# Performance work log

Hardware: AMD Instinct MI355X
Metric: run time of the kernel (lower is better)

## Reference

```python
import jax, jax.numpy as jnp
import numpy as np

B, U, V = 4, 64, 256
IN_DIM, STATE_DIM, CODE_DIM = 768, 768, 384
NUM_HEADS, HEAD_DIM = 8, 64
INNER = NUM_HEADS * HEAD_DIM  # 512
SCALE = HEAD_DIM ** 0.5


def _ln(x, g, b, eps=1e-5):
    mu = jnp.mean(x, axis=-1, keepdims=True)
    var = jnp.var(x, axis=-1, keepdims=True)
    return (x - mu) * jax.lax.rsqrt(var + eps) * g + b


def setup_inputs() -> dict:
    key = jax.random.key(0)
    ks = jax.random.split(key, 12)
    def w(k, shape, s=0.02):
        return jax.random.normal(k, shape, jnp.float32) * s
    return {
        "receiver_states": jax.random.normal(ks[0], (B, U, STATE_DIM), jnp.float32),
        "receiver_codes": jax.random.normal(ks[1], (B, U, CODE_DIM), jnp.float32),
        "sender_states": jax.random.normal(ks[2], (B, V, IN_DIM), jnp.float32),
        "ln_r_g": jnp.ones((STATE_DIM,), jnp.float32),
        "ln_r_b": jnp.zeros((STATE_DIM,), jnp.float32),
        "ln_s_g": jnp.ones((IN_DIM,), jnp.float32),
        "ln_s_b": jnp.zeros((IN_DIM,), jnp.float32),
        "Wq": w(ks[3], (STATE_DIM, INNER)), "bq": jnp.zeros((INNER,), jnp.float32), "Wmq": w(ks[4], (CODE_DIM, STATE_DIM)),
        "Wk": w(ks[5], (IN_DIM, INNER)),   "bk": jnp.zeros((INNER,), jnp.float32), "Wmk": w(ks[6], (CODE_DIM, IN_DIM)),
        "Wv": w(ks[7], (IN_DIM, INNER)),   "bv": jnp.zeros((INNER,), jnp.float32), "Wmv": w(ks[8], (CODE_DIM, IN_DIM)),
        "We": w(ks[9], (INNER, STATE_DIM)), "be": jnp.zeros((STATE_DIM,), jnp.float32), "Wme": w(ks[10], (CODE_DIM, INNER)),
        "gamma": jnp.ones((STATE_DIM,), jnp.float32),  # LayerScale, init 1.0
    }


def reference(receiver_states, receiver_codes, sender_states,
              ln_r_g, ln_r_b, ln_s_g, ln_s_b,
              Wq, bq, Wmq, Wk, bk, Wmk, Wv, bv, Wmv, We, be, Wme, gamma):
    r = _ln(receiver_states, ln_r_g, ln_r_b)   # (b,u,ds)
    s = _ln(sender_states, ln_s_g, ln_s_b)     # (b,v,di)
    # ModFC: y = (x * (1 + ctx @ Wm)) @ W + b  (code-conditioned input modulation)
    q = (r * (1.0 + receiver_codes @ Wmq)) @ Wq + bq          # (b,u,inner)
    mk = 1.0 + receiver_codes @ Wmk                           # (b,u,di)
    mv = 1.0 + receiver_codes @ Wmv                           # (b,u,di)
    xs = s[:, :, None, :]                                     # (b,v,1,di)
    k = (xs * mk[:, None, :, :]) @ Wk + bk                    # (b,v,u,inner)
    v = (xs * mv[:, None, :, :]) @ Wv + bv                    # (b,v,u,inner)
    qh = q.reshape(B, U, NUM_HEADS, HEAD_DIM)
    kh = k.reshape(B, V, U, NUM_HEADS, HEAD_DIM)
    vh = v.reshape(B, V, U, NUM_HEADS, HEAD_DIM)
    scores = jnp.einsum('buhc,bvuhc->bhuv', qh, kh) / SCALE   # (b,h,u,v)
    weights = jax.nn.softmax(scores, axis=-1)
    msg = jnp.einsum('bhuv,bvuhc->buhc', weights, vh).reshape(B, U, INNER)
    out = (msg * (1.0 + receiver_codes @ Wme)) @ We + be      # exit ModFC -> (b,u,ds)
    out = out * gamma                                         # LayerScale
    return receiver_states + out                              # residual
```

## Files before the change

kernel.cpp:

```cpp
#include <hip/hip_runtime.h>


#define DD 768
#define CDIM 384
#define NH 8
#define HD 64
#define INNER 512
#define VV 256

typedef unsigned short u16;

__device__ __forceinline__ void fma4(float4& a, float s, const float4& b) {
  a.x += s * b.x; a.y += s * b.y; a.z += s * b.z; a.w += s * b.w;
}

__device__ __forceinline__ float4 bexp(uint2 u) {
  float4 r;
  r.x = __uint_as_float(u.x << 16);
  r.y = __uint_as_float(u.x & 0xffff0000u);
  r.z = __uint_as_float(u.y << 16);
  r.w = __uint_as_float(u.y & 0xffff0000u);
  return r;
}

__device__ __forceinline__ u16 f2b(float v) {
  return (u16)((__float_as_uint(v) + 0x8000u) >> 16);
}

template <int K, int NS>
__device__ __forceinline__ void gcore(const float* __restrict__ A0, int lda,
                                      const float* __restrict__ Bp,
                                      float4& a0, float4& a1, float4& a2,
                                      float4& a3) {
  float4 b0[8], b1[8];
#pragma unroll
  for (int i = 0; i < 8; i++) b0[i] = *(const float4*)(Bp + (size_t)i * NS);
  const float* Bq = Bp + (size_t)8 * NS;
#pragma unroll 1
  for (int kk = 0; kk < K; kk += 16) {
#pragma unroll
    for (int i = 0; i < 8; i++) b1[i] = *(const float4*)(Bq + (size_t)i * NS);
    Bq += (size_t)8 * NS;
#pragma unroll
    for (int c = 0; c < 2; c++) {
      int kb = kk + c * 4;
      float4 f0 = *(const float4*)(A0 + kb);
      float4 f1 = *(const float4*)(A0 + lda + kb);
      float4 f2 = *(const float4*)(A0 + 2 * lda + kb);
      float4 f3 = *(const float4*)(A0 + 3 * lda + kb);
      float4 bv;
      bv = b0[c*4+0]; fma4(a0,f0.x,bv); fma4(a1,f1.x,bv); fma4(a2,f2.x,bv); fma4(a3,f3.x,bv);
      bv = b0[c*4+1]; fma4(a0,f0.y,bv); fma4(a1,f1.y,bv); fma4(a2,f2.y,bv); fma4(a3,f3.y,bv);
      bv = b0[c*4+2]; fma4(a0,f0.z,bv); fma4(a1,f1.z,bv); fma4(a2,f2.z,bv); fma4(a3,f3.z,bv);
      bv = b0[c*4+3]; fma4(a0,f0.w,bv); fma4(a1,f1.w,bv); fma4(a2,f2.w,bv); fma4(a3,f3.w,bv);
    }
    if (kk + 16 < K) {
#pragma unroll
      for (int i = 0; i < 8; i++) b0[i] = *(const float4*)(Bq + (size_t)i * NS);
      Bq += (size_t)8 * NS;
    }
#pragma unroll
    for (int c = 0; c < 2; c++) {
      int kb = kk + 8 + c * 4;
      float4 f0 = *(const float4*)(A0 + kb);
      float4 f1 = *(const float4*)(A0 + lda + kb);
      float4 f2 = *(const float4*)(A0 + 2 * lda + kb);
      float4 f3 = *(const float4*)(A0 + 3 * lda + kb);
      float4 bv;
      bv = b1[c*4+0]; fma4(a0,f0.x,bv); fma4(a1,f1.x,bv); fma4(a2,f2.x,bv); fma4(a3,f3.x,bv);
      bv = b1[c*4+1]; fma4(a0,f0.y,bv); fma4(a1,f1.y,bv); fma4(a2,f2.y,bv); fma4(a3,f3.y,bv);
      bv = b1[c*4+2]; fma4(a0,f0.z,bv); fma4(a1,f1.z,bv); fma4(a2,f2.z,bv); fma4(a3,f3.z,bv);
      bv = b1[c*4+3]; fma4(a0,f0.w,bv); fma4(a1,f1.w,bv); fma4(a2,f2.w,bv); fma4(a3,f3.w,bv);
    }
  }
}

template <int K, int NS>
__device__ __forceinline__ void gcoreb(const float* __restrict__ A0, int lda,
                                       const u16* __restrict__ Bp,
                                       float4& a0, float4& a1, float4& a2,
                                       float4& a3) {
  uint2 b0[8], b1[8];
#pragma unroll
  for (int i = 0; i < 8; i++) b0[i] = *(const uint2*)(Bp + (size_t)i * NS);
  const u16* Bq = Bp + (size_t)8 * NS;
#pragma unroll 1
  for (int kk = 0; kk < K; kk += 16) {
#pragma unroll
    for (int i = 0; i < 8; i++) b1[i] = *(const uint2*)(Bq + (size_t)i * NS);
    Bq += (size_t)8 * NS;
#pragma unroll
    for (int c = 0; c < 2; c++) {
      int kb = kk + c * 4;
      float4 f0 = *(const float4*)(A0 + kb);
      float4 f1 = *(const float4*)(A0 + lda + kb);
      float4 f2 = *(const float4*)(A0 + 2 * lda + kb);
      float4 f3 = *(const float4*)(A0 + 3 * lda + kb);
      float4 bv;
      bv = bexp(b0[c*4+0]); fma4(a0,f0.x,bv); fma4(a1,f1.x,bv); fma4(a2,f2.x,bv); fma4(a3,f3.x,bv);
      bv = bexp(b0[c*4+1]); fma4(a0,f0.y,bv); fma4(a1,f1.y,bv); fma4(a2,f2.y,bv); fma4(a3,f3.y,bv);
      bv = bexp(b0[c*4+2]); fma4(a0,f0.z,bv); fma4(a1,f1.z,bv); fma4(a2,f2.z,bv); fma4(a3,f3.z,bv);
      bv = bexp(b0[c*4+3]); fma4(a0,f0.w,bv); fma4(a1,f1.w,bv); fma4(a2,f2.w,bv); fma4(a3,f3.w,bv);
    }
    if (kk + 16 < K) {
#pragma unroll
      for (int i = 0; i < 8; i++) b0[i] = *(const uint2*)(Bq + (size_t)i * NS);
      Bq += (size_t)8 * NS;
    }
#pragma unroll
    for (int c = 0; c < 2; c++) {
      int kb = kk + 8 + c * 4;
      float4 f0 = *(const float4*)(A0 + kb);
      float4 f1 = *(const float4*)(A0 + lda + kb);
      float4 f2 = *(const float4*)(A0 + 2 * lda + kb);
      float4 f3 = *(const float4*)(A0 + 3 * lda + kb);
      float4 bv;
      bv = bexp(b1[c*4+0]); fma4(a0,f0.x,bv); fma4(a1,f1.x,bv); fma4(a2,f2.x,bv); fma4(a3,f3.x,bv);
      bv = bexp(b1[c*4+1]); fma4(a0,f0.y,bv); fma4(a1,f1.y,bv); fma4(a2,f2.y,bv); fma4(a3,f3.y,bv);
      bv = bexp(b1[c*4+2]); fma4(a0,f0.z,bv); fma4(a1,f1.z,bv); fma4(a2,f2.z,bv); fma4(a3,f3.z,bv);
      bv = bexp(b1[c*4+3]); fma4(a0,f0.w,bv); fma4(a1,f1.w,bv); fma4(a2,f2.w,bv); fma4(a3,f3.w,bv);
    }
  }
}


__global__ __launch_bounds__(256) void k_s0(
    const float* __restrict__ Wmq, const float* __restrict__ Wmk,
    const float* __restrict__ Wmv, const float* __restrict__ Wme,
    const float* __restrict__ Wq, const float* __restrict__ Wk,
    const float* __restrict__ Wv, const float* __restrict__ We,
    u16* __restrict__ bw) {
  __shared__ float TL[64 * 65];
  int bid = blockIdx.x, t = threadIdx.x;
  if (bid < 96) {
    int d0 = (bid >> 3) * 64, c0 = (bid & 7) * 64;
    int j = t & 63, i0 = t >> 6;
#pragma unroll
    for (int p = 0; p < 16; p++) {
      int i = p * 4 + i0;
      TL[i * 65 + j] = Wk[(size_t)(d0 + i) * INNER + c0 + j];
    }
    __syncthreads();
    u16* dst = bw + 2260992;
#pragma unroll
    for (int p = 0; p < 16; p++) {
      int i = p * 4 + i0;
      dst[(size_t)(c0 + i) * DD + d0 + j] = f2b(TL[j * 65 + i]);
    }
  } else {
    for (int idx = (bid - 96) * 256 + t; idx < 565248; idx += 1184 * 256) {
      const float* src; u16* dst; int off;
      if (idx < 73728)       { src = Wmq; dst = bw;           off = idx; }
      else if (idx < 147456) { src = Wmk; dst = bw + 294912;  off = idx - 73728; }
      else if (idx < 221184) { src = Wmv; dst = bw + 589824;  off = idx - 147456; }
      else if (idx < 270336) { src = Wme; dst = bw + 884736;  off = idx - 221184; }
      else if (idx < 368640) { src = Wq;  dst = bw + 1081344; off = idx - 270336; }
      else if (idx < 466944) { src = Wv;  dst = bw + 1474560; off = idx - 368640; }
      else                   { src = We;  dst = bw + 1867776; off = idx - 466944; }
      float4 v = *(const float4*)(src + (size_t)off * 4);
      ushort4 o;
      o.x = f2b(v.x); o.y = f2b(v.y); o.z = f2b(v.z); o.w = f2b(v.w);
      *(ushort4*)(dst + (size_t)off * 4) = o;
    }
  }
}

__global__ __launch_bounds__(256, 2) void k_s1(
    const float* __restrict__ ss, const float* __restrict__ rs,
    const float* __restrict__ g_s, const float* __restrict__ b_s,
    const float* __restrict__ g_r, const float* __restrict__ b_r,
    const float* __restrict__ codes, const u16* __restrict__ bw,
    float* __restrict__ s_ln, float* __restrict__ r_ln,
    float* __restrict__ cp) {
  __shared__ __align__(16) float SB[6400];
  int bid = blockIdx.x, t = threadIdx.x;
  if (bid < 176) {
    int nc = bid % 11, mb = bid / 11;
    int base = nc * 256;
    const u16* W; int N, colW;
    if (base < 768)       { W = bw;          N = DD;    colW = base; }
    else if (base < 1536) { W = bw + 294912; N = DD;    colW = base - 768; }
    else if (base < 2304) { W = bw + 589824; N = DD;    colW = base - 1536; }
    else                  { W = bw + 884736; N = INNER; colW = base - 2304; }
    int m0 = mb * 16;
#pragma unroll
    for (int p = 0; p < 24; p++) {
      int idx = p * 256 + t, r = idx / 384, k = idx % 384;
      SB[idx] = codes[(size_t)(m0 + r) * CDIM + k];
    }
    __syncthreads();
    int kl = t & 63, wid = t >> 6;
    const float* A0 = SB + (wid * 4) * 384;
    float4 a0 = {0,0,0,0}, a1 = {0,0,0,0}, a2 = {0,0,0,0}, a3 = {0,0,0,0};
    if (N == DD)
      gcoreb<384, DD>(A0, 384, W + colW + 4 * kl, a0, a1, a2, a3);
    else
      gcoreb<384, INNER>(A0, 384, W + colW + 4 * kl, a0, a1, a2, a3);
    int m = m0 + wid * 4, gcol = base + 4 * kl;
    *(float4*)(cp + (size_t)m * 2816 + gcol) = a0;
    *(float4*)(cp + (size_t)(m + 1) * 2816 + gcol) = a1;
    *(float4*)(cp + (size_t)(m + 2) * 2816 + gcol) = a2;
    *(float4*)(cp + (size_t)(m + 3) * 2816 + gcol) = a3;
  } else {
    int rr = bid - 176;
    const float *x, *g, *bb; float* y; int r;
    if (rr < 1024) { x = ss; g = g_s; bb = b_s; y = s_ln; r = rr; }
    else           { x = rs; g = g_r; bb = b_r; y = r_ln; r = rr - 1024; }
    const float* xr = x + (size_t)r * DD;
    float v0 = xr[t], v1 = xr[t + 256], v2 = xr[t + 512];
    float s = v0 + v1 + v2, sq = v0 * v0 + v1 * v1 + v2 * v2;
    for (int o = 32; o > 0; o >>= 1) {
      s += __shfl_down(s, o, 64); sq += __shfl_down(sq, o, 64);
    }
    int wid = t >> 6, lane = t & 63;
    if (lane == 0) { SB[wid] = s; SB[wid + 4] = sq; }
    __syncthreads();
    float sum = SB[0] + SB[1] + SB[2] + SB[3];
    float ssq = SB[4] + SB[5] + SB[6] + SB[7];
    float mu = sum * (1.0f / 768.0f);
    float var = ssq * (1.0f / 768.0f) - mu * mu;
    float rstd = rsqrtf(var + 1e-5f);
    float* yr = y + (size_t)r * DD;
    yr[t]       = (v0 - mu) * rstd * g[t]       + bb[t];
    yr[t + 256] = (v1 - mu) * rstd * g[t + 256] + bb[t + 256];
    yr[t + 512] = (v2 - mu) * rstd * g[t + 512] + bb[t + 512];
  }
}

__global__ __launch_bounds__(256, 2) void k_s2(
    const float* __restrict__ s_ln, const float* __restrict__ r_ln,
    const float* __restrict__ cp, const u16* __restrict__ bw,
    float* __restrict__ sT, float* __restrict__ qp) {
  __shared__ __align__(16) float SB[4160];
  int bid = blockIdx.x, t = threadIdx.x;
  if (bid < 128) {
    int ks = bid & 3, t2 = bid >> 2, nc = t2 & 1, mb = t2 >> 1;
    int m0 = mb * 16, col0 = nc * 256, k0 = ks * 192;
#pragma unroll
    for (int p = 0; p < 12; p++) {
      int idx = p * 256 + t, r = idx / 192, k = idx % 192;
      int d = k0 + k;
      float mqv = cp[(size_t)(m0 + r) * 2816 + d] + 1.0f;
      SB[idx] = r_ln[(size_t)(m0 + r) * DD + d] * mqv;
    }
    __syncthreads();
    int kl = t & 63, wid = t >> 6;
    int col = col0 + 4 * kl;
    const float* A0 = SB + (wid * 4) * 192;
    float4 a0 = {0,0,0,0}, a1 = {0,0,0,0}, a2 = {0,0,0,0}, a3 = {0,0,0,0};
    gcoreb<192, INNER>(A0, 192, bw + 1081344 + (size_t)k0 * INNER + col,
                       a0, a1, a2, a3);
    int m = m0 + wid * 4;
    float* dst = qp + (size_t)ks * (256 * INNER);
    *(float4*)(dst + (size_t)m * INNER + col) = a0;
    *(float4*)(dst + (size_t)(m + 1) * INNER + col) = a1;
    *(float4*)(dst + (size_t)(m + 2) * INNER + col) = a2;
    *(float4*)(dst + (size_t)(m + 3) * INNER + col) = a3;
  } else {
    int tid = bid - 128;
    int vt = tid & 3, dt = (tid >> 2) % 12, b = tid / 48;
    int v0 = vt * 64, d0 = dt * 64;
    int j = t & 63, i0 = t >> 6;
#pragma unroll
    for (int p = 0; p < 16; p++) {
      int i = p * 4 + i0;
      SB[i * 65 + j] = s_ln[(size_t)(b * VV + v0 + i) * DD + d0 + j];
    }
    __syncthreads();
#pragma unroll
    for (int p = 0; p < 16; p++) {
      int i = p * 4 + i0;
      sT[((size_t)b * DD + d0 + i) * VV + v0 + j] = SB[j * 65 + i];
    }
  }
}

__global__ __launch_bounds__(256, 2) void k_s3(
    const float* __restrict__ qp, const float* __restrict__ bq,
    const u16* __restrict__ bw, const float* __restrict__ cp,
    const float* __restrict__ bk, float* __restrict__ qm,
    float* __restrict__ qbk) {
  __shared__ __align__(16) float SB[1024];
  int bid = blockIdx.x, t = threadIdx.x;
  if (bid < 384) {
    int h = bid & 7, dc = (bid >> 3) % 3, mb = bid / 24;
    int m0 = mb * 16;
#pragma unroll
    for (int p = 0; p < 4; p++) {
      int idx = p * 256 + t, r = idx >> 6, c = idx & 63;
      int i = h * HD + c;
      size_t off = (size_t)(m0 + r) * INNER + i;
      SB[idx] = qp[off] + qp[131072 + off] + qp[262144 + off] +
                qp[393216 + off] + bq[i];
    }
    __syncthreads();
    int kl = t & 63, wid = t >> 6;
    int col = dc * 256 + 4 * kl;
    const float* A0 = SB + (wid * 4) * HD;
    float4 a0 = {0,0,0,0}, a1 = {0,0,0,0}, a2 = {0,0,0,0}, a3 = {0,0,0,0};
    gcoreb<64, DD>(A0, HD, bw + 2260992 + (size_t)(h * HD) * DD + col,
                   a0, a1, a2, a3);
#pragma unroll
    for (int j = 0; j < 4; j++) {
      float4 a = (j == 0) ? a0 : (j == 1) ? a1 : (j == 2) ? a2 : a3;
      int m = m0 + wid * 4 + j;
      const float* mkp = cp + (size_t)m * 2816 + 768 + col;
      float4 o = {a.x * (mkp[0] + 1.0f), a.y * (mkp[1] + 1.0f),
                  a.z * (mkp[2] + 1.0f), a.w * (mkp[3] + 1.0f)};
      *(float4*)(qm + ((size_t)m * NH + h) * DD + col) = o;
    }
  } else {
    int m = bid - 384;
    size_t off = (size_t)m * INNER;
    SB[t] = (qp[off + t] + qp[131072 + off + t] + qp[262144 + off + t] +
             qp[393216 + off + t] + bq[t]) * bk[t];
    int t2 = t + 256;
    SB[t2] = (qp[off + t2] + qp[131072 + off + t2] + qp[262144 + off + t2] +
              qp[393216 + off + t2] + bq[t2]) * bk[t2];
    __syncthreads();
    if (t < 8) {
      float a = 0.f;
      for (int c = 0; c < HD; c++) a += SB[t * HD + c];
      qbk[m * NH + t] = a;
    }
  }
}

__global__ __launch_bounds__(256, 2) void k_s4(
    const float* __restrict__ qm, const float* __restrict__ sT,
    float* __restrict__ scp) {
  __shared__ __align__(16) float SB[3072];
  int bid = blockIdx.x, t = threadIdx.x;
  int ks = bid & 3, b = (bid >> 2) & 3, mb = bid >> 4;
  int gi0 = b * 512 + mb * 16, k0 = ks * 192;
#pragma unroll
  for (int p = 0; p < 12; p++) {
    int idx = p * 256 + t, r = idx / 192, k = idx % 192;
    SB[idx] = qm[(size_t)(gi0 + r) * DD + k0 + k];
  }
  __syncthreads();
  int kl = t & 63, wid = t >> 6;
  int col = 4 * kl;
  const float* A0 = SB + (wid * 4) * 192;
  float4 a0 = {0,0,0,0}, a1 = {0,0,0,0}, a2 = {0,0,0,0}, a3 = {0,0,0,0};
  gcore<192, VV>(A0, 192, sT + ((size_t)b * DD + k0) * VV + col, a0, a1, a2, a3);
  int gi = gi0 + wid * 4;
  float* dst = scp + (size_t)ks * (2048 * VV);
  *(float4*)(dst + (size_t)gi * VV + col) = a0;
  *(float4*)(dst + (size_t)(gi + 1) * VV + col) = a1;
  *(float4*)(dst + (size_t)(gi + 2) * VV + col) = a2;
  *(float4*)(dst + (size_t)(gi + 3) * VV + col) = a3;
}

__global__ __launch_bounds__(256, 2) void k_s5(
    const float* __restrict__ scp, const float* __restrict__ qbk,
    const float* __restrict__ s_ln, const float* __restrict__ cp,
    float* __restrict__ wsm) {
  __shared__ __align__(16) float SB[4096];
  int bid = blockIdx.x, t = threadIdx.x;
  int dc = bid % 3, up = (bid / 3) % 32, b = bid / 96;
  int gi0 = b * 512 + up * 16;
#pragma unroll
  for (int p = 0; p < 16; p++) {
    int idx = p * 256 + t, r = idx >> 8, c = idx & 255;
    size_t o = (size_t)(gi0 + r) * VV + c;
    float v = scp[o] + scp[524288 + o] + scp[1048576 + o] + scp[1572864 + o];
    int m = b * 64 + up * 2 + (r >> 3), h = r & 7;
    SB[idx] = (v + qbk[m * NH + h]) * 0.125f;
  }
  __syncthreads();
  int wid = t >> 6, lane = t & 63;
#pragma unroll
  for (int j = 0; j < 4; j++) {
    int r = wid * 4 + j;
    float x0 = SB[r * 256 + lane],       x1 = SB[r * 256 + lane + 64];
    float x2 = SB[r * 256 + lane + 128], x3 = SB[r * 256 + lane + 192];
    float mx = fmaxf(fmaxf(x0, x1), fmaxf(x2, x3));
    for (int o = 1; o < 64; o <<= 1) mx = fmaxf(mx, __shfl_xor(mx, o, 64));
    float e0 = __expf(x0 - mx), e1 = __expf(x1 - mx);
    float e2 = __expf(x2 - mx), e3 = __expf(x3 - mx);
    float sm = e0 + e1 + e2 + e3;
    for (int o = 1; o < 64; o <<= 1) sm += __shfl_xor(sm, o, 64);
    float rinv = 1.0f / sm;
    SB[r * 256 + lane] = e0 * rinv;       SB[r * 256 + lane + 64] = e1 * rinv;
    SB[r * 256 + lane + 128] = e2 * rinv; SB[r * 256 + lane + 192] = e3 * rinv;
  }
  __syncthreads();
  int kl = t & 63;
  int col = dc * 256 + 4 * kl;
  const float* A0 = SB + (wid * 4) * 256;
  float4 a0 = {0,0,0,0}, a1 = {0,0,0,0}, a2 = {0,0,0,0}, a3 = {0,0,0,0};
  gcore<VV, DD>(A0, 256, s_ln + (size_t)(b * VV) * DD + col, a0, a1, a2, a3);
#pragma unroll
  for (int j = 0; j < 4; j++) {
    float4 a = (j == 0) ? a0 : (j == 1) ? a1 : (j == 2) ? a2 : a3;
    int r = wid * 4 + j;
    int ul = r >> 3, h = r & 7, m = b * 64 + up * 2 + ul;
    const float* mvp = cp + (size_t)m * 2816 + 1536 + col;
    float4 o = {a.x * (mvp[0] + 1.0f), a.y * (mvp[1] + 1.0f),
                a.z * (mvp[2] + 1.0f), a.w * (mvp[3] + 1.0f)};
    *(float4*)(wsm + ((size_t)h * 256 + m) * DD + col) = o;
  }
}

__global__ __launch_bounds__(256, 2) void k_s6(
    const float* __restrict__ wsm, const u16* __restrict__ bw,
    float* __restrict__ mmp) {
  __shared__ __align__(16) float SB[6400];
  int bid = blockIdx.x, t = threadIdx.x;
  int hp = bid & 1, ks = (bid >> 1) & 7, mb = bid >> 4;
  int h0 = hp * 4, m0 = mb * 16, k0 = ks * 96;
#pragma unroll
  for (int p = 0; p < 24; p++) {
    int idx = p * 256 + t;
    int e = idx / 1536, rem = idx % 1536, r = rem / 96, k = rem % 96;
    SB[e * 1540 + r * 96 + k] =
        wsm[((size_t)(h0 + e) * 256 + m0 + r) * DD + k0 + k];
  }
  __syncthreads();
  int kl = t & 63, wid = t >> 6;
  int hs = kl >> 4, c4 = 4 * (kl & 15);
  int colg = h0 * HD + hs * HD + c4;
  const float* A0 = SB + hs * 1540 + (wid * 4) * 96;
  float4 a0 = {0,0,0,0}, a1 = {0,0,0,0}, a2 = {0,0,0,0}, a3 = {0,0,0,0};
  gcoreb<96, INNER>(A0, 96, bw + 1474560 + (size_t)k0 * INNER + colg,
                    a0, a1, a2, a3);
  float* dst = mmp + (size_t)ks * (256 * INNER);
  int m = m0 + wid * 4;
  *(float4*)(dst + (size_t)m * INNER + colg) = a0;
  *(float4*)(dst + (size_t)(m + 1) * INNER + colg) = a1;
  *(float4*)(dst + (size_t)(m + 2) * INNER + colg) = a2;
  *(float4*)(dst + (size_t)(m + 3) * INNER + colg) = a3;
}

__global__ __launch_bounds__(256, 2) void k_s7(
    const float* __restrict__ mmp, const float* __restrict__ bvv,
    const float* __restrict__ cp, const u16* __restrict__ bw,
    float* __restrict__ op) {
  __shared__ __align__(16) float SB[1024];
  int bid = blockIdx.x, t = threadIdx.x;
  int ks = bid & 7, dc = (bid >> 3) % 3, mb = bid / 24;
  int m0 = mb * 16, k0 = ks * 64;
#pragma unroll
  for (int p = 0; p < 4; p++) {
    int idx = p * 256 + t, r = idx >> 6, k = idx & 63;
    int i = k0 + k;
    size_t off = (size_t)(m0 + r) * INNER + i;
    float v = mmp[off] + mmp[131072 + off] + mmp[262144 + off] +
              mmp[393216 + off] + mmp[524288 + off] + mmp[655360 + off] +
              mmp[786432 + off] + mmp[917504 + off];
    float mev = cp[(size_t)(m0 + r) * 2816 + 2304 + i] + 1.0f;
    SB[idx] = (v + bvv[i]) * mev;
  }
  __syncthreads();
  int kl = t & 63, wid = t >> 6;
  int col = dc * 256 + 4 * kl;
  const float* A0 = SB + (wid * 4) * 64;
  float4 a0 = {0,0,0,0}, a1 = {0,0,0,0}, a2 = {0,0,0,0}, a3 = {0,0,0,0};
  gcoreb<64, DD>(A0, 64, bw + 1867776 + (size_t)k0 * DD + col, a0, a1, a2, a3);
  float* dst = op + (size_t)ks * (256 * DD);
  int m = m0 + wid * 4;
  *(float4*)(dst + (size_t)m * DD + col) = a0;
  *(float4*)(dst + (size_t)(m + 1) * DD + col) = a1;
  *(float4*)(dst + (size_t)(m + 2) * DD + col) = a2;
  *(float4*)(dst + (size_t)(m + 3) * DD + col) = a3;
}

__global__ __launch_bounds__(256) void k_s8(
    const float* __restrict__ op, const float* __restrict__ be,
    const float* __restrict__ gamma, const float* __restrict__ rs,
    float* __restrict__ outp) {
  int m = blockIdx.x, t = threadIdx.x;
#pragma unroll
  for (int j = 0; j < 3; j++) {
    int d = t + j * 256;
    size_t off = (size_t)m * DD + d;
    float v = op[off] + op[196608 + off] + op[393216 + off] +
              op[589824 + off] + op[786432 + off] + op[983040 + off] +
              op[1179648 + off] + op[1376256 + off];
    outp[off] = rs[off] + (v + be[d]) * gamma[d];
  }
}

extern "C" void kernel_launch(void* const* d_in, const int* in_sizes, int n_in,
                              void* d_out, int out_size, void* d_ws, size_t ws_size,
                              hipStream_t stream) {
  const float* rs     = (const float*)d_in[0];
  const float* codes  = (const float*)d_in[1];
  const float* ss     = (const float*)d_in[2];
  const float* ln_r_g = (const float*)d_in[3];
  const float* ln_r_b = (const float*)d_in[4];
  const float* ln_s_g = (const float*)d_in[5];
  const float* ln_s_b = (const float*)d_in[6];
  const float* Wq  = (const float*)d_in[7];
  const float* bq  = (const float*)d_in[8];
  const float* Wmq = (const float*)d_in[9];
  const float* Wk  = (const float*)d_in[10];
  const float* bk  = (const float*)d_in[11];
  const float* Wmk = (const float*)d_in[12];
  const float* Wv  = (const float*)d_in[13];
  const float* bv  = (const float*)d_in[14];
  const float* Wmv = (const float*)d_in[15];
  const float* We  = (const float*)d_in[16];
  const float* be  = (const float*)d_in[17];
  const float* Wme = (const float*)d_in[18];
  const float* gamma = (const float*)d_in[19];

  float* w = (float*)d_ws;
  float* s_ln = w;
  float* r_ln = w + 786432;
  float* qp   = w + 1376256;
  float* sT   = w + 1900544;
  float* cp   = w + 2686976;
  float* qbk  = w + 3407872;
  float* qm   = w + 3409920;
  float* scp  = w + 4982784;
  float* wsm  = qm;
  float* mmp  = r_ln;
  float* op   = scp;
  u16*   bw   = (u16*)(w + 7079936);

  k_s0<<<dim3(1280), 256, 0, stream>>>(Wmq, Wmk, Wmv, Wme, Wq, Wk, Wv, We, bw);
  k_s1<<<dim3(1456), 256, 0, stream>>>(ss, rs, ln_s_g, ln_s_b, ln_r_g, ln_r_b,
                                       codes, bw, s_ln, r_ln, cp);
  k_s2<<<dim3(320), 256, 0, stream>>>(s_ln, r_ln, cp, bw, sT, qp);
  k_s3<<<dim3(640), 256, 0, stream>>>(qp, bq, bw, cp, bk, qm, qbk);
  k_s4<<<dim3(512), 256, 0, stream>>>(qm, sT, scp);
  k_s5<<<dim3(384), 256, 0, stream>>>(scp, qbk, s_ln, cp, wsm);
  k_s6<<<dim3(256), 256, 0, stream>>>(wsm, bw, mmp);
  k_s7<<<dim3(384), 256, 0, stream>>>(mmp, bv, cp, bw, op);
  k_s8<<<dim3(256), 256, 0, stream>>>(op, be, gamma, rs, (float*)d_out);
}
```

Measured before the change: 204.7 us.

## Halve per-block row tiles and fold weight conversion into first kernel

Each GEMM-style kernel now computes 2 rows per wave instead of 4, doubling the grid sizes of the stages to put more blocks on the many CUs. The separate weight-to-bf16 conversion kernel is merged into k_s1, and the code-modulation GEMM now reads fp32 weights directly and stores 1+x, so later stages drop their +1.0. This removes a launch and a dependency, but each block gets less register reuse of the loaded B vectors and more redundant B traffic.

```diff
diff --git a/kernel.cpp b/kernel.cpp
--- a/kernel.cpp
+++ b/kernel.cpp
@@ -28,10 +28,9 @@
 }
 
 template <int K, int NS>
-__device__ __forceinline__ void gcore(const float* __restrict__ A0, int lda,
-                                      const float* __restrict__ Bp,
-                                      float4& a0, float4& a1, float4& a2,
-                                      float4& a3) {
+__device__ __forceinline__ void gcore2(const float* __restrict__ A0, int lda,
+                                       const float* __restrict__ Bp,
+                                       float4& a0, float4& a1) {
   float4 b0[8], b1[8];
 #pragma unroll
   for (int i = 0; i < 8; i++) b0[i] = *(const float4*)(Bp + (size_t)i * NS);
@@ -46,13 +45,11 @@
       int kb = kk + c * 4;
       float4 f0 = *(const float4*)(A0 + kb);
       float4 f1 = *(const float4*)(A0 + lda + kb);
-      float4 f2 = *(const float4*)(A0 + 2 * lda + kb);
-      float4 f3 = *(const float4*)(A0 + 3 * lda + kb);
       float4 bv;
-      bv = b0[c*4+0]; fma4(a0,f0.x,bv); fma4(a1,f1.x,bv); fma4(a2,f2.x,bv); fma4(a3,f3.x,bv);
-      bv = b0[c*4+1]; fma4(a0,f0.y,bv); fma4(a1,f1.y,bv); fma4(a2,f2.y,bv); fma4(a3,f3.y,bv);
-      bv = b0[c*4+2]; fma4(a0,f0.z,bv); fma4(a1,f1.z,bv); fma4(a2,f2.z,bv); fma4(a3,f3.z,bv);
-      bv = b0[c*4+3]; fma4(a0,f0.w,bv); fma4(a1,f1.w,bv); fma4(a2,f2.w,bv); fma4(a3,f3.w,bv);
+      bv = b0[c*4+0]; fma4(a0, f0.x, bv); fma4(a1, f1.x, bv);
+      bv = b0[c*4+1]; fma4(a0, f0.y, bv); fma4(a1, f1.y, bv);
+      bv = b0[c*4+2]; fma4(a0, f0.z, bv); fma4(a1, f1.z, bv);
+      bv = b0[c*4+3]; fma4(a0, f0.w, bv); fma4(a1, f1.w, bv);
     }
     if (kk + 16 < K) {
 #pragma unroll
@@ -64,22 +61,19 @@
       int kb = kk + 8 + c * 4;
       float4 f0 = *(const float4*)(A0 + kb);
       float4 f1 = *(const float4*)(A0 + lda + kb);
-      float4 f2 = *(const float4*)(A0 + 2 * lda + kb);
-      float4 f3 = *(const float4*)(A0 + 3 * lda + kb);
       float4 bv;
-      bv = b1[c*4+0]; fma4(a0,f0.x,bv); fma4(a1,f1.x,bv); fma4(a2,f2.x,bv); fma4(a3,f3.x,bv);
-      bv = b1[c*4+1]; fma4(a0,f0.y,bv); fma4(a1,f1.y,bv); fma4(a2,f2.y,bv); fma4(a3,f3.y,bv);
-      bv = b1[c*4+2]; fma4(a0,f0.z,bv); fma4(a1,f1.z,bv); fma4(a2,f2.z,bv); fma4(a3,f3.z,bv);
-      bv = b1[c*4+3]; fma4(a0,f0.w,bv); fma4(a1,f1.w,bv); fma4(a2,f2.w,bv); fma4(a3,f3.w,bv);
+      bv = b1[c*4+0]; fma4(a0, f0.x, bv); fma4(a1, f1.x, bv);
+      bv = b1[c*4+1]; fma4(a0, f0.y, bv); fma4(a1, f1.y, bv);
+      bv = b1[c*4+2]; fma4(a0, f0.z, bv); fma4(a1, f1.z, bv);
+      bv = b1[c*4+3]; fma4(a0, f0.w, bv); fma4(a1, f1.w, bv);
     }
   }
 }
 
 template <int K, int NS>
-__device__ __forceinline__ void gcoreb(const float* __restrict__ A0, int lda,
-                                       const u16* __restrict__ Bp,
-                                       float4& a0, float4& a1, float4& a2,
-                                       float4& a3) {
+__device__ __forceinline__ void gcore2b(const float* __restrict__ A0, int lda,
+                                        const u16* __restrict__ Bp,
+                                        float4& a0, float4& a1) {
   uint2 b0[8], b1[8];
 #pragma unroll
   for (int i = 0; i < 8; i++) b0[i] = *(const uint2*)(Bp + (size_t)i * NS);
@@ -94,13 +88,11 @@
       int kb = kk + c * 4;
       float4 f0 = *(const float4*)(A0 + kb);
       float4 f1 = *(const float4*)(A0 + lda + kb);
-      float4 f2 = *(const float4*)(A0 + 2 * lda + kb);
-      float4 f3 = *(const float4*)(A0 + 3 * lda + kb);
       float4 bv;
-      bv = bexp(b0[c*4+0]); fma4(a0,f0.x,bv); fma4(a1,f1.x,bv); fma4(a2,f2.x,bv); fma4(a3,f3.x,bv);
-      bv = bexp(b0[c*4+1]); fma4(a0,f0.y,bv); fma4(a1,f1.y,bv); fma4(a2,f2.y,bv); fma4(a3,f3.y,bv);
-      bv = bexp(b0[c*4+2]); fma4(a0,f0.z,bv); fma4(a1,f1.z,bv); fma4(a2,f2.z,bv); fma4(a3,f3.z,bv);
-      bv = bexp(b0[c*4+3]); fma4(a0,f0.w,bv); fma4(a1,f1.w,bv); fma4(a2,f2.w,bv); fma4(a3,f3.w,bv);
+      bv = bexp(b0[c*4+0]); fma4(a0, f0.x, bv); fma4(a1, f1.x, bv);
+      bv = bexp(b0[c*4+1]); fma4(a0, f0.y, bv); fma4(a1, f1.y, bv);
+      bv = bexp(b0[c*4+2]); fma4(a0, f0.z, bv); fma4(a1, f1.z, bv);
+      bv = bexp(b0[c*4+3]); fma4(a0, f0.w, bv); fma4(a1, f1.w, bv);
     }
     if (kk + 16 < K) {
 #pragma unroll
@@ -112,97 +104,85 @@
       int kb = kk + 8 + c * 4;
       float4 f0 = *(const float4*)(A0 + kb);
       float4 f1 = *(const float4*)(A0 + lda + kb);
-      float4 f2 = *(const float4*)(A0 + 2 * lda + kb);
-      float4 f3 = *(const float4*)(A0 + 3 * lda + kb);
       float4 bv;
-      bv = bexp(b1[c*4+0]); fma4(a0,f0.x,bv); fma4(a1,f1.x,bv); fma4(a2,f2.x,bv); fma4(a3,f3.x,bv);
-      bv = bexp(b1[c*4+1]); fma4(a0,f0.y,bv); fma4(a1,f1.y,bv); fma4(a2,f2.y,bv); fma4(a3,f3.y,bv);
-      bv = bexp(b1[c*4+2]); fma4(a0,f0.z,bv); fma4(a1,f1.z,bv); fma4(a2,f2.z,bv); fma4(a3,f3.z,bv);
-      bv = bexp(b1[c*4+3]); fma4(a0,f0.w,bv); fma4(a1,f1.w,bv); fma4(a2,f2.w,bv); fma4(a3,f3.w,bv);
-    }
-  }
-}
-
-
-__global__ __launch_bounds__(256) void k_s0(
-    const float* __restrict__ Wmq, const float* __restrict__ Wmk,
-    const float* __restrict__ Wmv, const float* __restrict__ Wme,
-    const float* __restrict__ Wq, const float* __restrict__ Wk,
-    const float* __restrict__ Wv, const float* __restrict__ We,
-    u16* __restrict__ bw) {
-  __shared__ float TL[64 * 65];
-  int bid = blockIdx.x, t = threadIdx.x;
-  if (bid < 96) {
-    int d0 = (bid >> 3) * 64, c0 = (bid & 7) * 64;
+      bv = bexp(b1[c*4+0]); fma4(a0, f0.x, bv); fma4(a1, f1.x, bv);
+      bv = bexp(b1[c*4+1]); fma4(a0, f0.y, bv); fma4(a1, f1.y, bv);
+      bv = bexp(b1[c*4+2]); fma4(a0, f0.z, bv); fma4(a1, f1.z, bv);
+      bv = bexp(b1[c*4+3]); fma4(a0, f0.w, bv); fma4(a1, f1.w, bv);
+    }
+  }
+}
+
+
+__global__ __launch_bounds__(256, 2) void k_s1(
+    const float* __restrict__ ss, const float* __restrict__ rs,
+    const float* __restrict__ g_s, const float* __restrict__ b_s,
+    const float* __restrict__ g_r, const float* __restrict__ b_r,
+    const float* __restrict__ codes, const float* __restrict__ Wmq,
+    const float* __restrict__ Wmk, const float* __restrict__ Wmv,
+    const float* __restrict__ Wme, const float* __restrict__ Wk,
+    const float* __restrict__ Wq, const float* __restrict__ Wv,
+    const float* __restrict__ We,
+    float* __restrict__ s_ln, float* __restrict__ r_ln,
+    float* __restrict__ cp, u16* __restrict__ bw) {
+  __shared__ __align__(16) float SB[4160];
+  int bid = blockIdx.x, t = threadIdx.x;
+  if (bid < 352) {
+    int nc = bid % 11, mb = bid / 11;
+    int base = nc * 256;
+    const float* W; int N, colW;
+    if (base < 768)       { W = Wmq; N = DD;    colW = base; }
+    else if (base < 1536) { W = Wmk; N = DD;    colW = base - 768; }
+    else if (base < 2304) { W = Wmv; N = DD;    colW = base - 1536; }
+    else                  { W = Wme; N = INNER; colW = base - 2304; }
+    int m0 = mb * 8;
+#pragma unroll
+    for (int p = 0; p < 12; p++) {
+      int idx = p * 256 + t, r = idx / 384, k = idx % 384;
+      SB[idx] = codes[(size_t)(m0 + r) * CDIM + k];
+    }
+    __syncthreads();
+    int kl = t & 63, wid = t >> 6;
+    const float* A0 = SB + (wid * 2) * 384;
+    float4 a0 = {0,0,0,0}, a1 = {0,0,0,0};
+    if (N == DD)
+      gcore2<384, DD>(A0, 384, W + colW + 4 * kl, a0, a1);
+    else
+      gcore2<384, INNER>(A0, 384, W + colW + 4 * kl, a0, a1);
+    int m = m0 + wid * 2, gcol = base + 4 * kl;
+    float4 o0 = {1.f + a0.x, 1.f + a0.y, 1.f + a0.z, 1.f + a0.w};
+    float4 o1 = {1.f + a1.x, 1.f + a1.y, 1.f + a1.z, 1.f + a1.w};
+    *(float4*)(cp + (size_t)m * 2816 + gcol) = o0;
+    *(float4*)(cp + (size_t)(m + 1) * 2816 + gcol) = o1;
+  } else if (bid < 448) {
+    int tid = bid - 352;
+    int d0 = (tid >> 3) * 64, c0 = (tid & 7) * 64;
     int j = t & 63, i0 = t >> 6;
 #pragma unroll
     for (int p = 0; p < 16; p++) {
       int i = p * 4 + i0;
-      TL[i * 65 + j] = Wk[(size_t)(d0 + i) * INNER + c0 + j];
-    }
-    __syncthreads();
-    u16* dst = bw + 2260992;
+      SB[i * 65 + j] = Wk[(size_t)(d0 + i) * INNER + c0 + j];
+    }
+    __syncthreads();
+    u16* dst = bw + 1179648;
 #pragma unroll
     for (int p = 0; p < 16; p++) {
       int i = p * 4 + i0;
-      dst[(size_t)(c0 + i) * DD + d0 + j] = f2b(TL[j * 65 + i]);
-    }
-  } else {
-    for (int idx = (bid - 96) * 256 + t; idx < 565248; idx += 1184 * 256) {
+      dst[(size_t)(c0 + i) * DD + d0 + j] = f2b(SB[j * 65 + i]);
+    }
+  } else if (bid < 896) {
+    for (int idx = (bid - 448) * 256 + t; idx < 294912; idx += 448 * 256) {
       const float* src; u16* dst; int off;
-      if (idx < 73728)       { src = Wmq; dst = bw;           off = idx; }
-      else if (idx < 147456) { src = Wmk; dst = bw + 294912;  off = idx - 73728; }
-      else if (idx < 221184) { src = Wmv; dst = bw + 589824;  off = idx - 147456; }
-      else if (idx < 270336) { src = Wme; dst = bw + 884736;  off = idx - 221184; }
-      else if (idx < 368640) { src = Wq;  dst = bw + 1081344; off = idx - 270336; }
-      else if (idx < 466944) { src = Wv;  dst = bw + 1474560; off = idx - 368640; }
-      else                   { src = We;  dst = bw + 1867776; off = idx - 466944; }
+      if (idx < 98304)       { src = Wq; dst = bw;          off = idx; }
+      else if (idx < 196608) { src = Wv; dst = bw + 393216; off = idx - 98304; }
+      else                   { src = We; dst = bw + 786432; off = idx - 196608; }
       float4 v = *(const float4*)(src + (size_t)off * 4);
       ushort4 o;
       o.x = f2b(v.x); o.y = f2b(v.y); o.z = f2b(v.z); o.w = f2b(v.w);
       *(ushort4*)(dst + (size_t)off * 4) = o;
     }
-  }
-}
-
-__global__ __launch_bounds__(256, 2) void k_s1(
-    const float* __restrict__ ss, const float* __restrict__ rs,
-    const float* __restrict__ g_s, const float* __restrict__ b_s,
-    const float* __restrict__ g_r, const float* __restrict__ b_r,
-    const float* __restrict__ codes, const u16* __restrict__ bw,
-    float* __restrict__ s_ln, float* __restrict__ r_ln,
-    float* __restrict__ cp) {
-  __shared__ __align__(16) float SB[6400];
-  int bid = blockIdx.x, t = threadIdx.x;
-  if (bid < 176) {
-    int nc = bid % 11, mb = bid / 11;
-    int base = nc * 256;
-    const u16* W; int N, colW;
-    if (base < 768)       { W = bw;          N = DD;    colW = base; }
-    else if (base < 1536) { W = bw + 294912; N = DD;    colW = base - 768; }
-    else if (base < 2304) { W = bw + 589824; N = DD;    colW = base - 1536; }
-    else                  { W = bw + 884736; N = INNER; colW = base - 2304; }
-    int m0 = mb * 16;
-#pragma unroll
-    for (int p = 0; p < 24; p++) {
-      int idx = p * 256 + t, r = idx / 384, k = idx % 384;
-      SB[idx] = codes[(size_t)(m0 + r) * CDIM + k];
-    }
-    __syncthreads();
-    int kl = t & 63, wid = t >> 6;
-    const float* A0 = SB + (wid * 4) * 384;
-    float4 a0 = {0,0,0,0}, a1 = {0,0,0,0}, a2 = {0,0,0,0}, a3 = {0,0,0,0};
-    if (N == DD)
-      gcoreb<384, DD>(A0, 384, W + colW + 4 * kl, a0, a1, a2, a3);
-    else
-      gcoreb<384, INNER>(A0, 384, W + colW + 4 * kl, a0, a1, a2, a3);
-    int m = m0 + wid * 4, gcol = base + 4 * kl;
-    *(float4*)(cp + (size_t)m * 2816 + gcol) = a0;
-    *(float4*)(cp + (size_t)(m + 1) * 2816 + gcol) = a1;
-    *(float4*)(cp + (size_t)(m + 2) * 2816 + gcol) = a2;
-    *(float4*)(cp + (size_t)(m + 3) * 2816 + gcol) = a3;
   } else {
-    int rr = bid - 176;
+    int rr = bid - 896;
     const float *x, *g, *bb; float* y; int r;
     if (rr < 1024) { x = ss; g = g_s; bb = b_s; y = s_ln; r = rr; }
     else           { x = rs; g = g_r; bb = b_r; y = r_ln; r = rr - 1024; }
@@ -233,31 +213,27 @@
     float* __restrict__ sT, float* __restrict__ qp) {
   __shared__ __align__(16) float SB[4160];
   int bid = blockIdx.x, t = threadIdx.x;
-  if (bid < 128) {
+  if (bid < 256) {
     int ks = bid & 3, t2 = bid >> 2, nc = t2 & 1, mb = t2 >> 1;
-    int m0 = mb * 16, col0 = nc * 256, k0 = ks * 192;
-#pragma unroll
-    for (int p = 0; p < 12; p++) {
+    int m0 = mb * 8, col0 = nc * 256, k0 = ks * 192;
+#pragma unroll
+    for (int p = 0; p < 6; p++) {
       int idx = p * 256 + t, r = idx / 192, k = idx % 192;
       int d = k0 + k;
-      float mqv = cp[(size_t)(m0 + r) * 2816 + d] + 1.0f;
-      SB[idx] = r_ln[(size_t)(m0 + r) * DD + d] * mqv;
+      SB[idx] = r_ln[(size_t)(m0 + r) * DD + d] * cp[(size_t)(m0 + r) * 2816 + d];
     }
     __syncthreads();
     int kl = t & 63, wid = t >> 6;
     int col = col0 + 4 * kl;
-    const float* A0 = SB + (wid * 4) * 192;
-    float4 a0 = {0,0,0,0}, a1 = {0,0,0,0}, a2 = {0,0,0,0}, a3 = {0,0,0,0};
-    gcoreb<192, INNER>(A0, 192, bw + 1081344 + (size_t)k0 * INNER + col,
-                       a0, a1, a2, a3);
-    int m = m0 + wid * 4;
+    const float* A0 = SB + (wid * 2) * 192;
+    float4 a0 = {0,0,0,0}, a1 = {0,0,0,0};
+    gcore2b<192, INNER>(A0, 192, bw + (size_t)k0 * INNER + col, a0, a1);
+    int m = m0 + wid * 2;
     float* dst = qp + (size_t)ks * (256 * INNER);
     *(float4*)(dst + (size_t)m * INNER + col) = a0;
     *(float4*)(dst + (size_t)(m + 1) * INNER + col) = a1;
-    *(float4*)(dst + (size_t)(m + 2) * INNER + col) = a2;
-    *(float4*)(dst + (size_t)(m + 3) * INNER + col) = a3;
   } else {
-    int tid = bid - 128;
+    int tid = bid - 256;
     int vt = tid & 3, dt = (tid >> 2) % 12, b = tid / 48;
     int v0 = vt * 64, d0 = dt * 64;
     int j = t & 63, i0 = t >> 6;
@@ -280,13 +256,13 @@
     const u16* __restrict__ bw, const float* __restrict__ cp,
     const float* __restrict__ bk, float* __restrict__ qm,
     float* __restrict__ qbk) {
-  __shared__ __align__(16) float SB[1024];
-  int bid = blockIdx.x, t = threadIdx.x;
-  if (bid < 384) {
+  __shared__ __align__(16) float SB[512];
+  int bid = blockIdx.x, t = threadIdx.x;
+  if (bid < 768) {
     int h = bid & 7, dc = (bid >> 3) % 3, mb = bid / 24;
-    int m0 = mb * 16;
-#pragma unroll
-    for (int p = 0; p < 4; p++) {
+    int m0 = mb * 8;
+#pragma unroll
+    for (int p = 0; p < 2; p++) {
       int idx = p * 256 + t, r = idx >> 6, c = idx & 63;
       int i = h * HD + c;
       size_t off = (size_t)(m0 + r) * INNER + i;
@@ -296,31 +272,32 @@
     __syncthreads();
     int kl = t & 63, wid = t >> 6;
     int col = dc * 256 + 4 * kl;
-    const float* A0 = SB + (wid * 4) * HD;
-    float4 a0 = {0,0,0,0}, a1 = {0,0,0,0}, a2 = {0,0,0,0}, a3 = {0,0,0,0};
-    gcoreb<64, DD>(A0, HD, bw + 2260992 + (size_t)(h * HD) * DD + col,
-                   a0, a1, a2, a3);
-#pragma unroll
-    for (int j = 0; j < 4; j++) {
-      float4 a = (j == 0) ? a0 : (j == 1) ? a1 : (j == 2) ? a2 : a3;
-      int m = m0 + wid * 4 + j;
+    const float* A0 = SB + (wid * 2) * HD;
+    float4 a0 = {0,0,0,0}, a1 = {0,0,0,0};
+    gcore2b<64, DD>(A0, HD, bw + 1179648 + (size_t)(h * HD) * DD + col, a0, a1);
+#pragma unroll
+    for (int j = 0; j < 2; j++) {
+      float4 a = (j == 0) ? a0 : a1;
+      int m = m0 + wid * 2 + j;
       const float* mkp = cp + (size_t)m * 2816 + 768 + col;
-      float4 o = {a.x * (mkp[0] + 1.0f), a.y * (mkp[1] + 1.0f),
-                  a.z * (mkp[2] + 1.0f), a.w * (mkp[3] + 1.0f)};
+      float4 o = {a.x * mkp[0], a.y * mkp[1], a.z * mkp[2], a.w * mkp[3]};
       *(float4*)(qm + ((size_t)m * NH + h) * DD + col) = o;
     }
   } else {
-    int m = bid - 384;
+    int m = bid - 768;
     size_t off = (size_t)m * INNER;
-    SB[t] = (qp[off + t] + qp[131072 + off + t] + qp[262144 + off + t] +
-             qp[393216 + off + t] + bq[t]) * bk[t];
+    SB[t & 255] = 0.f;
+    float va = (qp[off + t] + qp[131072 + off + t] + qp[262144 + off + t] +
+                qp[393216 + off + t] + bq[t]) * bk[t];
     int t2 = t + 256;
-    SB[t2] = (qp[off + t2] + qp[131072 + off + t2] + qp[262144 + off + t2] +
-              qp[393216 + off + t2] + bq[t2]) * bk[t2];
+    float vb = (qp[off + t2] + qp[131072 + off + t2] + qp[262144 + off + t2] +
+                qp[393216 + off + t2] + bq[t2]) * bk[t2];
+    __shared__ float RED[512];
+    RED[t] = va; RED[t2] = vb;
     __syncthreads();
     if (t < 8) {
       float a = 0.f;
-      for (int c = 0; c < HD; c++) a += SB[t * HD + c];
+      for (int c = 0; c < HD; c++) a += RED[t * HD + c];
       qbk[m * NH + t] = a;
     }
   }
@@ -329,52 +306,49 @@
 __global__ __launch_bounds__(256, 2) void k_s4(
     const float* __restrict__ qm, const float* __restrict__ sT,
     float* __restrict__ scp) {
-  __shared__ __align__(16) float SB[3072];
+  __shared__ __align__(16) float SB[1536];
   int bid = blockIdx.x, t = threadIdx.x;
   int ks = bid & 3, b = (bid >> 2) & 3, mb = bid >> 4;
-  int gi0 = b * 512 + mb * 16, k0 = ks * 192;
-#pragma unroll
-  for (int p = 0; p < 12; p++) {
+  int gi0 = b * 512 + mb * 8, k0 = ks * 192;
+#pragma unroll
+  for (int p = 0; p < 6; p++) {
     int idx = p * 256 + t, r = idx / 192, k = idx % 192;
     SB[idx] = qm[(size_t)(gi0 + r) * DD + k0 + k];
   }
   __syncthreads();
   int kl = t & 63, wid = t >> 6;
   int col = 4 * kl;
-  const float* A0 = SB + (wid * 4) * 192;
-  float4 a0 = {0,0,0,0}, a1 = {0,0,0,0}, a2 = {0,0,0,0}, a3 = {0,0,0,0};
-  gcore<192, VV>(A0, 192, sT + ((size_t)b * DD + k0) * VV + col, a0, a1, a2, a3);
-  int gi = gi0 + wid * 4;
+  const float* A0 = SB + (wid * 2) * 192;
+  float4 a0 = {0,0,0,0}, a1 = {0,0,0,0};
+  gcore2<192, VV>(A0, 192, sT + ((size_t)b * DD + k0) * VV + col, a0, a1);
+  int gi = gi0 + wid * 2;
   float* dst = scp + (size_t)ks * (2048 * VV);
   *(float4*)(dst + (size_t)gi * VV + col) = a0;
   *(float4*)(dst + (size_t)(gi + 1) * VV + col) = a1;
-  *(float4*)(dst + (size_t)(gi + 2) * VV + col) = a2;
-  *(float4*)(dst + (size_t)(gi + 3) * VV + col) = a3;
 }
 
 __global__ __launch_bounds__(256, 2) void k_s5(
     const float* __restrict__ scp, const float* __restrict__ qbk,
     const float* __restrict__ s_ln, const float* __restrict__ cp,
     float* __restrict__ wsm) {
-  __shared__ __align__(16) float SB[4096];
-  int bid = blockIdx.x, t = threadIdx.x;
-  int dc = bid % 3, up = (bid / 3) % 32, b = bid / 96;
-  int gi0 = b * 512 + up * 16;
-#pragma unroll
-  for (int p = 0; p < 16; p++) {
-    int idx = p * 256 + t, r = idx >> 8, c = idx & 255;
-    size_t o = (size_t)(gi0 + r) * VV + c;
+  __shared__ __align__(16) float SC[2048];
+  int bid = blockIdx.x, t = threadIdx.x;
+  int dc = bid % 3, u = (bid / 3) % 64, b = bid / 192;
+  int m = b * 64 + u, gi0 = b * 512 + u * 8;
+#pragma unroll
+  for (int p = 0; p < 8; p++) {
+    int idx = p * 256 + t, h = idx >> 8, c = idx & 255;
+    size_t o = (size_t)(gi0 + h) * VV + c;
     float v = scp[o] + scp[524288 + o] + scp[1048576 + o] + scp[1572864 + o];
-    int m = b * 64 + up * 2 + (r >> 3), h = r & 7;
-    SB[idx] = (v + qbk[m * NH + h]) * 0.125f;
+    SC[idx] = (v + qbk[m * NH + h]) * 0.125f;
   }
   __syncthreads();
   int wid = t >> 6, lane = t & 63;
 #pragma unroll
-  for (int j = 0; j < 4; j++) {
-    int r = wid * 4 + j;
-    float x0 = SB[r * 256 + lane],       x1 = SB[r * 256 + lane + 64];
-    float x2 = SB[r * 256 + lane + 128], x3 = SB[r * 256 + lane + 192];
+  for (int j = 0; j < 2; j++) {
+    int h = wid * 2 + j;
+    float x0 = SC[h * 256 + lane],       x1 = SC[h * 256 + lane + 64];
+    float x2 = SC[h * 256 + lane + 128], x3 = SC[h * 256 + lane + 192];
     float mx = fmaxf(fmaxf(x0, x1), fmaxf(x2, x3));
     for (int o = 1; o < 64; o <<= 1) mx = fmaxf(mx, __shfl_xor(mx, o, 64));
     float e0 = __expf(x0 - mx), e1 = __expf(x1 - mx);
@@ -382,23 +356,22 @@
     float sm = e0 + e1 + e2 + e3;
     for (int o = 1; o < 64; o <<= 1) sm += __shfl_xor(sm, o, 64);
     float rinv = 1.0f / sm;
-    SB[r * 256 + lane] = e0 * rinv;       SB[r * 256 + lane + 64] = e1 * rinv;
-    SB[r * 256 + lane + 128] = e2 * rinv; SB[r * 256 + lane + 192] = e3 * rinv;
+    SC[h * 256 + lane] = e0 * rinv;       SC[h * 256 + lane + 64] = e1 * rinv;
+    SC[h * 256 + lane + 128] = e2 * rinv; SC[h * 256 + lane + 192] = e3 * rinv;
   }
   __syncthreads();
   int kl = t & 63;
   int col = dc * 256 + 4 * kl;
-  const float* A0 = SB + (wid * 4) * 256;
-  float4 a0 = {0,0,0,0}, a1 = {0,0,0,0}, a2 = {0,0,0,0}, a3 = {0,0,0,0};
-  gcore<VV, DD>(A0, 256, s_ln + (size_t)(b * VV) * DD + col, a0, a1, a2, a3);
-#pragma unroll
-  for (int j = 0; j < 4; j++) {
-    float4 a = (j == 0) ? a0 : (j == 1) ? a1 : (j == 2) ? a2 : a3;
-    int r = wid * 4 + j;
-    int ul = r >> 3, h = r & 7, m = b * 64 + up * 2 + ul;
-    const float* mvp = cp + (size_t)m * 2816 + 1536 + col;
-    float4 o = {a.x * (mvp[0] + 1.0f), a.y * (mvp[1] + 1.0f),
-                a.z * (mvp[2] + 1.0f), a.w * (mvp[3] + 1.0f)};
+  const float* A0 = SC + (wid * 2) * 256;
+  float4 a0 = {0,0,0,0}, a1 = {0,0,0,0};
+  gcore2<VV, DD>(A0, 256, s_ln + (size_t)(b * VV) * DD + col, a0, a1);
+  const float* mvp = cp + (size_t)m * 2816 + 1536 + col;
+  float4 mv4 = {mvp[0], mvp[1], mvp[2], mvp[3]};
+#pragma unroll
+  for (int j = 0; j < 2; j++) {
+    float4 a = (j == 0) ? a0 : a1;
+    int h = wid * 2 + j;
+    float4 o = {a.x * mv4.x, a.y * mv4.y, a.z * mv4.z, a.w * mv4.w};
     *(float4*)(wsm + ((size_t)h * 256 + m) * DD + col) = o;
   }
 }
@@ -406,64 +379,58 @@
 __global__ __launch_bounds__(256, 2) void k_s6(
     const float* __restrict__ wsm, const u16* __restrict__ bw,
     float* __restrict__ mmp) {
-  __shared__ __align__(16) float SB[6400];
+  __shared__ __align__(16) float SB[3088];
   int bid = blockIdx.x, t = threadIdx.x;
   int hp = bid & 1, ks = (bid >> 1) & 7, mb = bid >> 4;
-  int h0 = hp * 4, m0 = mb * 16, k0 = ks * 96;
-#pragma unroll
-  for (int p = 0; p < 24; p++) {
+  int h0 = hp * 4, m0 = mb * 8, k0 = ks * 96;
+#pragma unroll
+  for (int p = 0; p < 12; p++) {
     int idx = p * 256 + t;
-    int e = idx / 1536, rem = idx % 1536, r = rem / 96, k = rem % 96;
-    SB[e * 1540 + r * 96 + k] =
+    int e = idx / 768, rem = idx % 768, r = rem / 96, k = rem % 96;
+    SB[e * 772 + r * 96 + k] =
         wsm[((size_t)(h0 + e) * 256 + m0 + r) * DD + k0 + k];
   }
   __syncthreads();
   int kl = t & 63, wid = t >> 6;
   int hs = kl >> 4, c4 = 4 * (kl & 15);
   int colg = h0 * HD + hs * HD + c4;
-  const float* A0 = SB + hs * 1540 + (wid * 4) * 96;
-  float4 a0 = {0,0,0,0}, a1 = {0,0,0,0}, a2 = {0,0,0,0}, a3 = {0,0,0,0};
-  gcoreb<96, INNER>(A0, 96, bw + 1474560 + (size_t)k0 * INNER + colg,
-                    a0, a1, a2, a3);
+  const float* A0 = SB + hs * 772 + (wid * 2) * 96;
+  float4 a0 = {0,0,0,0}, a1 = {0,0,0,0};
+  gcore2b<96, INNER>(A0, 96, bw + 393216 + (size_t)k0 * INNER + colg, a0, a1);
   float* dst = mmp + (size_t)ks * (256 * INNER);
-  int m = m0 + wid * 4;
+  int m = m0 + wid * 2;
   *(float4*)(dst + (size_t)m * INNER + colg) = a0;
   *(float4*)(dst + (size_t)(m + 1) * INNER + colg) = a1;
-  *(float4*)(dst + (size_t)(m + 2) * INNER + colg) = a2;
-  *(float4*)(dst + (size_t)(m + 3) * INNER + colg) = a3;
 }
 
 __global__ __launch_bounds__(256, 2) void k_s7(
     const float* __restrict__ mmp, const float* __restrict__ bvv,
     const float* __restrict__ cp, const u16* __restrict__ bw,
     float* __restrict__ op) {
-  __shared__ __align__(16) float SB[1024];
+  __shared__ __align__(16) float SB[512];
   int bid = blockIdx.x, t = threadIdx.x;
   int ks = bid & 7, dc = (bid >> 3) % 3, mb = bid / 24;
-  int m0 = mb * 16, k0 = ks * 64;
-#pragma unroll
-  for (int p = 0; p < 4; p++) {
+  int m0 = mb * 8, k0 = ks * 64;
+#pragma unroll
+  for (int p = 0; p < 2; p++) {
     int idx = p * 256 + t, r = idx >> 6, k = idx & 63;
     int i = k0 + k;
     size_t off = (size_t)(m0 + r) * INNER + i;
     float v = mmp[off] + mmp[131072 + off] + mmp[262144 + off] +
               mmp[393216 + off] + mmp[524288 + off] + mmp[655360 + off] +
               mmp[786432 + off] + mmp[917504 + off];
-    float mev = cp[(size_t)(m0 + r) * 2816 + 2304 + i] + 1.0f;
-    SB[idx] = (v + bvv[i]) * mev;
+    SB[idx] = (v + bvv[i]) * cp[(size_t)(m0 + r) * 2816 + 2304 + i];
   }
   __syncthreads();
   int kl = t & 63, wid = t >> 6;
   int col = dc * 256 + 4 * kl;
-  const float* A0 = SB + (wid * 4) * 64;
-  float4 a0 = {0,0,0,0}, a1 = {0,0,0,0}, a2 = {0,0,0,0}, a3 = {0,0,0,0};
-  gcoreb<64, DD>(A0, 64, bw + 1867776 + (size_t)k0 * DD + col, a0, a1, a2, a3);
+  const float* A0 = SB + (wid * 2) * 64;
+  float4 a0 = {0,0,0,0}, a1 = {0,0,0,0};
+  gcore2b<64, DD>(A0, 64, bw + 786432 + (size_t)k0 * DD + col, a0, a1);
   float* dst = op + (size_t)ks * (256 * DD);
-  int m = m0 + wid * 4;
+  int m = m0 + wid * 2;
   *(float4*)(dst + (size_t)m * DD + col) = a0;
   *(float4*)(dst + (size_t)(m + 1) * DD + col) = a1;
-  *(float4*)(dst + (size_t)(m + 2) * DD + col) = a2;
-  *(float4*)(dst + (size_t)(m + 3) * DD + col) = a3;
 }
 
 __global__ __launch_bounds__(256) void k_s8(
@@ -520,14 +487,14 @@
   float* op   = scp;
   u16*   bw   = (u16*)(w + 7079936);
 
-  k_s0<<<dim3(1280), 256, 0, stream>>>(Wmq, Wmk, Wmv, Wme, Wq, Wk, Wv, We, bw);
-  k_s1<<<dim3(1456), 256, 0, stream>>>(ss, rs, ln_s_g, ln_s_b, ln_r_g, ln_r_b,
-                                       codes, bw, s_ln, r_ln, cp);
-  k_s2<<<dim3(320), 256, 0, stream>>>(s_ln, r_ln, cp, bw, sT, qp);
-  k_s3<<<dim3(640), 256, 0, stream>>>(qp, bq, bw, cp, bk, qm, qbk);
-  k_s4<<<dim3(512), 256, 0, stream>>>(qm, sT, scp);
-  k_s5<<<dim3(384), 256, 0, stream>>>(scp, qbk, s_ln, cp, wsm);
-  k_s6<<<dim3(256), 256, 0, stream>>>(wsm, bw, mmp);
-  k_s7<<<dim3(384), 256, 0, stream>>>(mmp, bv, cp, bw, op);
+  k_s1<<<dim3(2176), 256, 0, stream>>>(ss, rs, ln_s_g, ln_s_b, ln_r_g, ln_r_b,
+                                       codes, Wmq, Wmk, Wmv, Wme, Wk, Wq, Wv,
+                                       We, s_ln, r_ln, cp, bw);
+  k_s2<<<dim3(448), 256, 0, stream>>>(s_ln, r_ln, cp, bw, sT, qp);
+  k_s3<<<dim3(1024), 256, 0, stream>>>(qp, bq, bw, cp, bk, qm, qbk);
+  k_s4<<<dim3(1024), 256, 0, stream>>>(qm, sT, scp);
+  k_s5<<<dim3(768), 256, 0, stream>>>(scp, qbk, s_ln, cp, wsm);
+  k_s6<<<dim3(512), 256, 0, stream>>>(wsm, bw, mmp);
+  k_s7<<<dim3(768), 256, 0, stream>>>(mmp, bv, cp, bw, op);
   k_s8<<<dim3(256), 256, 0, stream>>>(op, be, gamma, rs, (float*)d_out);
 }
```

Measured after the change: 219.0 us. +7.0%, slower.
